# Kernel optimization log

Measured on AMD Instinct MI355X. Metric: run time of the kernel, lower is better.

## Reference

```python
import math
import jax, jax.numpy as jnp
import numpy as np

B, T, D_MODEL, H, D = 2, 1024, 1024, 16, 64
NUM_LEVELS = int(math.ceil(math.log2(T + 1))) + 1  # 12 for max_seq_len=1024


def _fenwick_level(idx):
    return (idx & -idx).bit_length() - 1


def build_fenwick_masks(T, num_levels):
    """NumPy replica of the torch build_fenwick_masks; returns [L, T, T] float32."""
    j_to_nodes = {}
    for j in range(1, T + 1):
        nodes = []
        idx = j
        while idx <= T:
            nodes.append((idx, _fenwick_level(idx)))
            idx += idx & -idx
        j_to_nodes[j] = nodes
    t_to_query_nodes = {}
    for t in range(1, T + 1):
        s = set()
        idx = t
        while idx > 0:
            s.add(idx)
            idx -= idx & -idx
        t_to_query_nodes[t] = s
    masks = np.zeros((num_levels, T, T), dtype=np.float32)
    for t in range(1, T + 1):
        qn = t_to_query_nodes[t]
        for j in range(1, t + 1):
            for node_idx, node_level in j_to_nodes[j]:
                if node_idx in qn:
                    masks[min(node_level, num_levels - 1), t - 1, j - 1] = 1.0
                    break
    return masks


def setup_inputs() -> dict:
    key = jax.random.key(0)
    ks = jax.random.split(key, 8)
    s = 0.02
    return {
        "x": jax.random.normal(ks[0], (B, T, D_MODEL), jnp.float32),
        "qw": jax.random.normal(ks[1], (D_MODEL, H * D), jnp.float32) * s,
        "qb": jnp.zeros((H * D,), jnp.float32),
        "kw": jax.random.normal(ks[2], (D_MODEL, H * D), jnp.float32) * s,
        "kb": jnp.zeros((H * D,), jnp.float32),
        "vw": jax.random.normal(ks[3], (D_MODEL, H * D), jnp.float32) * s,
        "vb": jnp.zeros((H * D,), jnp.float32),
        "lw": jax.random.normal(ks[4], (D_MODEL, H * NUM_LEVELS), jnp.float32) * s,
        "lb": jnp.zeros((H * NUM_LEVELS,), jnp.float32),
        "ow": jax.random.normal(ks[5], (H * D, D_MODEL), jnp.float32) * s,
        "ob": jnp.zeros((D_MODEL,), jnp.float32),
        "level_masks": jnp.asarray(build_fenwick_masks(T, NUM_LEVELS)),
    }


def reference(x, qw, qb, kw, kb, vw, vb, lw, lb, ow, ob, level_masks):
    b, t, _ = x.shape
    phi = lambda a: jax.nn.elu(a) + 1.0  # ELU+1 feature map
    # projections -> [B, H, T, D]
    Q = (x @ qw + qb).reshape(b, t, H, D).transpose(0, 2, 1, 3)
    K = (x @ kw + kb).reshape(b, t, H, D).transpose(0, 2, 1, 3)
    V = (x @ vw + vb).reshape(b, t, H, D).transpose(0, 2, 1, 3)
    Qp, Kp = phi(Q), phi(K)
    # per-level mixing weights: [B, H, T, L]
    logits = (x @ lw + lb).reshape(b, t, H, NUM_LEVELS).transpose(0, 2, 1, 3)
    w = jax.nn.softmax(logits, axis=-1)
    # scores are level-independent in the original; compute once
    S = jnp.einsum('bhid,bhjd->bhij', Qp, Kp)
    # sum_l w_l * mask_l folded into one weighted mask: [B, H, T, T]
    Mw = jnp.einsum('bhil,lij->bhij', w, level_masks)
    Sm = S * Mw
    num = jnp.einsum('bhij,bhjd->bhid', Sm, V)
    den = jnp.maximum(jnp.sum(Sm, axis=-1, keepdims=True), 1e-6)
    out = (num / den).transpose(0, 2, 1, 3).reshape(b, t, H * D)
    return out @ ow + ob
```

## Files before the change

kernel.cpp:

```cpp
#include <hip/hip_runtime.h>
#include <math.h>

typedef __bf16 bf16;
typedef __attribute__((ext_vector_type(4))) __bf16 bf16x4;
typedef __attribute__((ext_vector_type(8))) __bf16 bf16x8;
typedef __attribute__((ext_vector_type(4))) float f32x4;

#define B_SZ 2
#define T_SZ 1024
#define DM_SZ 1024
#define H_SZ 16
#define D_SZ 64
#define L_SZ 12
#define M_ROWS 2048
#define N_PAD 3328

__device__ __forceinline__ f32x4 mfma_16x16x32(bf16x8 a, bf16x8 b, f32x4 c) {
  return __builtin_amdgcn_mfma_f32_16x16x32_bf16(a, b, c, 0, 0, 0);
}

__device__ __forceinline__ void gload_lds16(const bf16* g, bf16* l) {
  __builtin_amdgcn_global_load_lds((const __attribute__((address_space(1))) void*)g,
                                   (__attribute__((address_space(3))) void*)l,
                                   16, 0, 0);
}

__global__ __launch_bounds__(256) void k_prep(
    const float* __restrict__ x, bf16* __restrict__ xb,
    const float* __restrict__ qw, const float* __restrict__ kw,
    const float* __restrict__ vw, const float* __restrict__ ow,
    const float* __restrict__ lw,
    bf16* __restrict__ wqkvT, bf16* __restrict__ owT) {
  const int z = blockIdx.z;
  const int t = threadIdx.x;
  if (z == 5) {
    const size_t base = ((size_t)blockIdx.y * 16 + blockIdx.x) * 8192 + t * 32;
#pragma unroll
    for (int u = 0; u < 4; ++u) {
      const float* p = x + base + u * 8;
      f32x4 a = *(const f32x4*)p;
      f32x4 b = *(const f32x4*)(p + 4);
      bf16x8 o;
#pragma unroll
      for (int e = 0; e < 4; ++e) { o[e] = (bf16)a[e]; o[e + 4] = (bf16)b[e]; }
      *(bf16x8*)(xb + base + u * 8) = o;
    }
    return;
  }
  __shared__ __align__(16) bf16 tile[64][66];
  const float* in; bf16* out; int C = 1024;
  if (z == 0)      { in = qw; out = wqkvT; }
  else if (z == 1) { in = kw; out = wqkvT + (size_t)1024 * DM_SZ; }
  else if (z == 2) { in = vw; out = wqkvT + (size_t)2048 * DM_SZ; }
  else if (z == 3) { in = ow; out = owT; }
  else             { in = lw; out = wqkvT + (size_t)3072 * DM_SZ; C = 192;
                     if (blockIdx.x >= 3) return; }
  const int tc = blockIdx.x * 64;
  const int tr = blockIdx.y * 64;
  const int r = t >> 2;
  const int c4 = (t & 3) << 4;
  const float* src = in + (size_t)(tr + r) * C + tc + c4;
  f32x4 f0 = *(const f32x4*)(src);
  f32x4 f1 = *(const f32x4*)(src + 4);
  f32x4 f2 = *(const f32x4*)(src + 8);
  f32x4 f3 = *(const f32x4*)(src + 12);
#pragma unroll
  for (int e = 0; e < 4; ++e) {
    tile[r][c4 + e]      = (bf16)f0[e];
    tile[r][c4 + 4 + e]  = (bf16)f1[e];
    tile[r][c4 + 8 + e]  = (bf16)f2[e];
    tile[r][c4 + 12 + e] = (bf16)f3[e];
  }
  __syncthreads();
  bf16x8 w0, w1;
#pragma unroll
  for (int e = 0; e < 8; ++e) { w0[e] = tile[c4 + e][r]; w1[e] = tile[c4 + 8 + e][r]; }
  bf16* dst = out + (size_t)(tc + r) * DM_SZ + tr + c4;
  *(bf16x8*)(dst) = w0;
  *(bf16x8*)(dst + 8) = w1;
}

__global__ __launch_bounds__(256) void k_gemm_qkvl(
    const bf16* __restrict__ A, const bf16* __restrict__ Wt,
    const float* __restrict__ qb, const float* __restrict__ kb,
    const float* __restrict__ vb, const float* __restrict__ lb,
    bf16* __restrict__ Qp, bf16* __restrict__ Kp,
    bf16* __restrict__ VTg, float* __restrict__ logit) {
  __shared__ __align__(16) char smem[34816];
  bf16* As = (bf16*)smem;
  bf16* Bs = As + 8192;
  const int nb = blockIdx.x * 128;
  const int mb = blockIdx.y * 128;
  const int t = threadIdx.x;
  const int wv = t >> 6;
  const int lane = t & 63;
  const int l16 = lane & 15;
  const int quad = lane >> 4;
  const int wm = (wv & 1) * 64;
  const int wn = (wv >> 1) * 64;

  const int trow = t >> 3;
  const int tcol = (t & 7) * 8;

  const f32x4 zero4 = {0.f, 0.f, 0.f, 0.f};
  f32x4 acc[4][4];
#pragma unroll
  for (int i = 0; i < 4; ++i)
#pragma unroll
    for (int j = 0; j < 4; ++j) acc[i][j] = zero4;

  const bf16* ag = A + (size_t)(mb + trow) * DM_SZ + tcol;
  const bf16* bg = Wt + (size_t)(nb + trow) * DM_SZ + tcol;

  for (int k0 = 0; k0 < DM_SZ; k0 += 64) {
    __syncthreads();
#pragma unroll
    for (int i = 0; i < 4; ++i)
      gload_lds16(ag + (size_t)i * 32 * DM_SZ + k0, As + i * 2048 + t * 8);
#pragma unroll
    for (int i = 0; i < 4; ++i)
      gload_lds16(bg + (size_t)i * 32 * DM_SZ + k0, Bs + i * 2048 + t * 8);
    __syncthreads();
#pragma unroll
    for (int ks = 0; ks < 2; ++ks) {
      bf16x8 af[4];
#pragma unroll
      for (int mi = 0; mi < 4; ++mi)
        af[mi] = *(const bf16x8*)(As + (wm + mi * 16 + l16) * 64 + ks * 32 + quad * 8);
#pragma unroll
      for (int ni = 0; ni < 4; ++ni) {
        bf16x8 bfr = *(const bf16x8*)(Bs + (wn + ni * 16 + l16) * 64 + ks * 32 + quad * 8);
#pragma unroll
        for (int mi = 0; mi < 4; ++mi)
          acc[mi][ni] = mfma_16x16x32(af[mi], bfr, acc[mi][ni]);
      }
    }
  }

  const int seg = nb >> 10;
  if (seg < 2) {
    const float* bias = seg == 0 ? qb : kb;
    bf16* outp = seg == 0 ? Qp : Kp;
    const int c0 = (nb & 1023) + wn;
#pragma unroll
    for (int ni = 0; ni < 4; ++ni) {
      const int col = c0 + ni * 16 + l16;
      const float bv = bias[col];
#pragma unroll
      for (int mi = 0; mi < 4; ++mi) {
#pragma unroll
        for (int r = 0; r < 4; ++r) {
          const int row = mb + wm + mi * 16 + quad * 4 + r;
          float v = acc[mi][ni][r] + bv;
          v = (v > 0.f) ? (v + 1.f) : __expf(v);
          outp[(size_t)row * DM_SZ + col] = (bf16)v;
        }
      }
    }
  } else if (seg == 2) {
    bf16* Trt = (bf16*)smem;
    const int cb = nb - 2048;
    __syncthreads();
#pragma unroll
    for (int ni = 0; ni < 4; ++ni) {
      const int nloc = wn + ni * 16 + l16;
      const float bv = vb[cb + nloc];
#pragma unroll
      for (int mi = 0; mi < 4; ++mi) {
        const int mloc = wm + mi * 16 + quad * 4;
        bf16x4 pk;
#pragma unroll
        for (int r = 0; r < 4; ++r) pk[r] = (bf16)(acc[mi][ni][r] + bv);
        *(bf16x4*)&Trt[nloc * 136 + mloc] = pk;
      }
    }
    __syncthreads();
    const int dn = t >> 1, ch = t & 1;
    const int bq = mb >> 10;
    const int m0g = mb & 1023;
    bf16* dst = VTg + ((size_t)(bq * 1024 + cb + dn)) * T_SZ + m0g + ch * 64;
    const bf16* srcl = Trt + dn * 136 + ch * 64;
#pragma unroll
    for (int e = 0; e < 8; ++e)
      *(bf16x8*)(dst + e * 8) = *(const bf16x8*)(srcl + e * 8);
  } else {
    const int lc0 = (nb - 3072) + wn;
#pragma unroll
    for (int ni = 0; ni < 4; ++ni) {
      const int lcol = lc0 + ni * 16 + l16;
      if (lcol < H_SZ * L_SZ) {
        const float bv = lb[lcol];
#pragma unroll
        for (int mi = 0; mi < 4; ++mi) {
#pragma unroll
          for (int r = 0; r < 4; ++r) {
            const int row = mb + wm + mi * 16 + quad * 4 + r;
            logit[(size_t)row * (H_SZ * L_SZ) + lcol] = acc[mi][ni][r] + bv;
          }
        }
      }
    }
  }
}

__global__ __launch_bounds__(256) void k_attn(const bf16* __restrict__ Qp,
                                              const bf16* __restrict__ Kp,
                                              const bf16* __restrict__ VTg,
                                              const float* __restrict__ Lg,
                                              bf16* __restrict__ O) {
  __shared__ __align__(16) bf16 Ks[64][80];
  __shared__ __align__(16) bf16 VTs[64][80];
  __shared__ __align__(16) bf16 Pl[4][16][80];
  __shared__ float Ws[64 * L_SZ];

  const int idx = blockIdx.x;
  const int s = idx >> 5;
  const int bh = idx & 31;
  const int it = (s < 8) ? (15 - s) : (s - 8);
  const int b = bh >> 4;
  const int h = bh & 15;
  const int i0 = it * 64;
  const int t = threadIdx.x;
  const int wv = t >> 6;
  const int lane = t & 63;
  const int l16 = lane & 15;
  const int quad = lane >> 4;
  const int m0 = wv * 16;

  const size_t base_bt = (size_t)b * T_SZ;

  const bf16* qptr = Qp + (base_bt + i0 + m0 + l16) * DM_SZ + h * 64 + quad * 8;
  const bf16x8 aq0 = *(const bf16x8*)(qptr);
  const bf16x8 aq1 = *(const bf16x8*)(qptr + 32);

  if (t < 64) {
    const float* lp = Lg + (base_bt + i0 + t) * (H_SZ * L_SZ) + h * L_SZ;
    float v[L_SZ];
    float m = -1e30f;
#pragma unroll
    for (int l = 0; l < L_SZ; ++l) { v[l] = lp[l]; m = fmaxf(m, v[l]); }
    float sum = 0.f;
#pragma unroll
    for (int l = 0; l < L_SZ; ++l) { v[l] = __expf(v[l] - m); sum += v[l]; }
    const float inv = 1.f / sum;
#pragma unroll
    for (int l = 0; l < L_SZ; ++l) Ws[t * L_SZ + l] = v[l] * inv;
  }

  const f32x4 zero4 = {0.f, 0.f, 0.f, 0.f};
  f32x4 accn[4];
#pragma unroll
  for (int tn = 0; tn < 4; ++tn) accn[tn] = zero4;
  float den[4] = {0.f, 0.f, 0.f, 0.f};

  const int sr = t >> 2;
  const int sc = (t & 3) << 4;
  const int il_base = m0 + quad * 4;

  const bf16* vtrow = VTg + ((size_t)bh * 64 + sr) * T_SZ;

  for (int jt = 0; jt <= it; ++jt) {
    const int j0 = jt * 64;
    const bf16* kpg = Kp + (base_bt + j0 + sr) * DM_SZ + h * 64 + sc;
    bf16x8 k0v = *(const bf16x8*)(kpg);
    bf16x8 k1v = *(const bf16x8*)(kpg + 8);
    const bf16* vpg = vtrow + j0 + sc;
    bf16x8 v0v = *(const bf16x8*)(vpg);
    bf16x8 v1v = *(const bf16x8*)(vpg + 8);
    __syncthreads();
    *(bf16x8*)&Ks[sr][sc] = k0v;
    *(bf16x8*)&Ks[sr][sc + 8] = k1v;
    *(bf16x8*)&VTs[sr][sc] = v0v;
    *(bf16x8*)&VTs[sr][sc + 8] = v1v;
    __syncthreads();

    f32x4 sacc[4];
#pragma unroll
    for (int tn = 0; tn < 4; ++tn) {
      sacc[tn] = zero4;
      bf16x8 bk0 = *(const bf16x8*)&Ks[tn * 16 + l16][quad * 8];
      bf16x8 bk1 = *(const bf16x8*)&Ks[tn * 16 + l16][32 + quad * 8];
      sacc[tn] = mfma_16x16x32(aq0, bk0, sacc[tn]);
      sacc[tn] = mfma_16x16x32(aq1, bk1, sacc[tn]);
    }

    if (jt < it) {
      const int lvlA = 6 + (31 - __clz((unsigned)(it ^ jt)));
      const int lvlB = 6 + (31 - __clz((unsigned)((it + 1) ^ jt)));
      float wrow[4];
#pragma unroll
      for (int r = 0; r < 4; ++r) {
        const int il = il_base + r;
        wrow[r] = Ws[il * L_SZ + ((il == 63) ? lvlB : lvlA)];
      }
#pragma unroll
      for (int tn = 0; tn < 4; ++tn) {
#pragma unroll
        for (int r = 0; r < 4; ++r) {
          const float p = sacc[tn][r] * wrow[r];
          den[r] += p;
          Pl[wv][quad * 4 + r][(tn * 16 + l16) ^ (quad << 4)] = (bf16)p;
        }
      }
    } else {
#pragma unroll
      for (int tn = 0; tn < 4; ++tn) {
#pragma unroll
        for (int r = 0; r < 4; ++r) {
          const int il = il_base + r;
          const int ig = i0 + il;
          const int jg = j0 + tn * 16 + l16;
          float p = 0.f;
          if (jg <= ig) {
            const int lvl = 31 - __clz((unsigned)((ig + 1) ^ jg));
            p = sacc[tn][r] * Ws[il * L_SZ + lvl];
          }
          den[r] += p;
          Pl[wv][quad * 4 + r][(tn * 16 + l16) ^ (quad << 4)] = (bf16)p;
        }
      }
    }

#pragma unroll
    for (int ks = 0; ks < 2; ++ks) {
      bf16x8 apf = *(const bf16x8*)&Pl[wv][l16][(ks * 32 + quad * 8) ^ ((l16 >> 2) << 4)];
#pragma unroll
      for (int tn = 0; tn < 4; ++tn) {
        bf16x8 bvf = *(const bf16x8*)&VTs[tn * 16 + l16][ks * 32 + quad * 8];
        accn[tn] = mfma_16x16x32(apf, bvf, accn[tn]);
      }
    }
  }

#pragma unroll
  for (int r = 0; r < 4; ++r) {
    float d = den[r];
    d += __shfl_xor(d, 1, 64);
    d += __shfl_xor(d, 2, 64);
    d += __shfl_xor(d, 4, 64);
    d += __shfl_xor(d, 8, 64);
    den[r] = fmaxf(d, 1e-6f);
  }

#pragma unroll
  for (int tn = 0; tn < 4; ++tn) {
#pragma unroll
    for (int r = 0; r < 4; ++r) {
      const int il = il_base + r;
      O[(base_bt + i0 + il) * DM_SZ + h * 64 + tn * 16 + l16] =
          (bf16)(accn[tn][r] / den[r]);
    }
  }
}

__global__ __launch_bounds__(256) void k_gemm_out(const bf16* __restrict__ A,
                                                  const bf16* __restrict__ Wt,
                                                  const float* __restrict__ ob,
                                                  float* __restrict__ out) {
  __shared__ __align__(16) bf16 As[64 * 64];
  __shared__ __align__(16) bf16 Bs[64 * 64];
  const int nb = blockIdx.x * 64;
  const int mb = blockIdx.y * 64;
  const int t = threadIdx.x;
  const int wv = t >> 6;
  const int lane = t & 63;
  const int l16 = lane & 15;
  const int quad = lane >> 4;
  const int wm = wv * 16;

  const int trow = t >> 3;
  const int tcol = (t & 7) * 8;

  const f32x4 zero4 = {0.f, 0.f, 0.f, 0.f};
  f32x4 acc[4];
#pragma unroll
  for (int j = 0; j < 4; ++j) acc[j] = zero4;

  const bf16* ag = A + (size_t)(mb + trow) * DM_SZ + tcol;
  const bf16* bg = Wt + (size_t)(nb + trow) * DM_SZ + tcol;

  for (int k0 = 0; k0 < DM_SZ; k0 += 64) {
    __syncthreads();
    gload_lds16(ag + k0, As + t * 8);
    gload_lds16(ag + (size_t)32 * DM_SZ + k0, As + 2048 + t * 8);
    gload_lds16(bg + k0, Bs + t * 8);
    gload_lds16(bg + (size_t)32 * DM_SZ + k0, Bs + 2048 + t * 8);
    __syncthreads();
#pragma unroll
    for (int ks = 0; ks < 2; ++ks) {
      bf16x8 af = *(const bf16x8*)(As + (wm + l16) * 64 + ks * 32 + quad * 8);
#pragma unroll
      for (int ni = 0; ni < 4; ++ni) {
        bf16x8 bfr = *(const bf16x8*)(Bs + (ni * 16 + l16) * 64 + ks * 32 + quad * 8);
        acc[ni] = mfma_16x16x32(af, bfr, acc[ni]);
      }
    }
  }
#pragma unroll
  for (int ni = 0; ni < 4; ++ni) {
    const int col = nb + ni * 16 + l16;
    const float bv = ob[col];
#pragma unroll
    for (int r = 0; r < 4; ++r) {
      const int row = mb + wm + quad * 4 + r;
      out[(size_t)row * DM_SZ + col] = acc[ni][r] + bv;
    }
  }
}

extern "C" void kernel_launch(void* const* d_in, const int* in_sizes, int n_in,
                              void* d_out, int out_size, void* d_ws, size_t ws_size,
                              hipStream_t stream) {
  (void)in_sizes; (void)n_in; (void)out_size; (void)ws_size;
  const float* x  = (const float*)d_in[0];
  const float* qw = (const float*)d_in[1];
  const float* qb = (const float*)d_in[2];
  const float* kw = (const float*)d_in[3];
  const float* kb = (const float*)d_in[4];
  const float* vw = (const float*)d_in[5];
  const float* vb = (const float*)d_in[6];
  const float* lw = (const float*)d_in[7];
  const float* lb = (const float*)d_in[8];
  const float* ow = (const float*)d_in[9];
  const float* ob = (const float*)d_in[10];

  char* ws = (char*)d_ws;
  size_t off = 0;
  auto alloc = [&](size_t bytes) -> char* {
    char* p = ws + off;
    off += (bytes + 255) & ~(size_t)255;
    return p;
  };
  bf16* xb     = (bf16*)alloc((size_t)M_ROWS * DM_SZ * 2);
  bf16* wqkvT  = (bf16*)alloc((size_t)N_PAD * DM_SZ * 2);
  bf16* owT    = (bf16*)alloc((size_t)DM_SZ * DM_SZ * 2);
  bf16* Qp     = (bf16*)alloc((size_t)M_ROWS * DM_SZ * 2);
  bf16* Kpb    = (bf16*)alloc((size_t)M_ROWS * DM_SZ * 2);
  bf16* VTg    = (bf16*)alloc((size_t)M_ROWS * DM_SZ * 2);
  bf16* attn   = (bf16*)alloc((size_t)M_ROWS * DM_SZ * 2);
  float* logit = (float*)alloc((size_t)M_ROWS * H_SZ * L_SZ * 4);

  const dim3 blk(256);
  k_prep<<<dim3(16, 16, 6), blk, 0, stream>>>(x, xb, qw, kw, vw, ow, lw, wqkvT, owT);
  k_gemm_qkvl<<<dim3(N_PAD / 128, M_ROWS / 128), blk, 0, stream>>>(
      xb, wqkvT, qb, kb, vb, lb, Qp, Kpb, VTg, logit);
  k_attn<<<dim3((T_SZ / 64) * B_SZ * H_SZ), blk, 0, stream>>>(Qp, Kpb, VTg, logit, attn);
  k_gemm_out<<<dim3(DM_SZ / 64, M_ROWS / 64), blk, 0, stream>>>(attn, owT, ob, (float*)d_out);
}
```

Before: 182.6 us.

## Fuse all stages into one cooperative persistent kernel with grid syncs

Merges the prep, QKV/logit GEMM, attention and output GEMM kernels into a single cooperative launch of 512 blocks, using grid.sync between phases and reusing one shared-memory buffer. The goal is to remove three kernel launch gaps and tail drains. The cost is that each phase is capped at 512 resident blocks, and work that was spread over more blocks is now looped or left idle (for example only 416 blocks run the GEMM). A fallback path launches the separate kernels if the cooperative launch fails.

```diff
diff --git a/kernel.cpp b/kernel.cpp
--- a/kernel.cpp
+++ b/kernel.cpp
@@ -1,5 +1,8 @@
 #include <hip/hip_runtime.h>
+#include <hip/hip_cooperative_groups.h>
 #include <math.h>
+
+namespace cg = cooperative_groups;
 
 typedef __bf16 bf16;
 typedef __attribute__((ext_vector_type(4))) __bf16 bf16x4;
@@ -14,6 +17,7 @@
 #define L_SZ 12
 #define M_ROWS 2048
 #define N_PAD 3328
+#define SMEM_BYTES 34816
 
 __device__ __forceinline__ f32x4 mfma_16x16x32(bf16x8 a, bf16x8 b, f32x4 c) {
   return __builtin_amdgcn_mfma_f32_16x16x32_bf16(a, b, c, 0, 0, 0);
@@ -25,40 +29,49 @@
                                    16, 0, 0);
 }
 
-__global__ __launch_bounds__(256) void k_prep(
-    const float* __restrict__ x, bf16* __restrict__ xb,
-    const float* __restrict__ qw, const float* __restrict__ kw,
-    const float* __restrict__ vw, const float* __restrict__ ow,
-    const float* __restrict__ lw,
-    bf16* __restrict__ wqkvT, bf16* __restrict__ owT) {
-  const int z = blockIdx.z;
-  const int t = threadIdx.x;
-  if (z == 5) {
-    const size_t base = ((size_t)blockIdx.y * 16 + blockIdx.x) * 8192 + t * 32;
-#pragma unroll
-    for (int u = 0; u < 4; ++u) {
-      const float* p = x + base + u * 8;
+struct Params {
+  const float *x, *qw, *kw, *vw, *ow, *lw;
+  const float *qb, *kb, *vb, *lb, *ob;
+  bf16 *xb, *wqkvT, *owT, *Qp, *Kp, *VTg, *attn;
+  float *logit;
+  float *out;
+};
+
+__device__ void prep_unit(int u, int t, char* smem, const Params& P) {
+  if (u >= 1328) return;
+  if (u >= 1072) {
+    const int cu = u - 1072;
+    const size_t base = (size_t)cu * 8192 + t * 32;
+#pragma unroll
+    for (int c = 0; c < 4; ++c) {
+      const float* p = P.x + base + c * 8;
       f32x4 a = *(const f32x4*)p;
       f32x4 b = *(const f32x4*)(p + 4);
       bf16x8 o;
 #pragma unroll
       for (int e = 0; e < 4; ++e) { o[e] = (bf16)a[e]; o[e + 4] = (bf16)b[e]; }
-      *(bf16x8*)(xb + base + u * 8) = o;
+      *(bf16x8*)(P.xb + base + c * 8) = o;
     }
     return;
   }
-  __shared__ __align__(16) bf16 tile[64][66];
-  const float* in; bf16* out; int C = 1024;
-  if (z == 0)      { in = qw; out = wqkvT; }
-  else if (z == 1) { in = kw; out = wqkvT + (size_t)1024 * DM_SZ; }
-  else if (z == 2) { in = vw; out = wqkvT + (size_t)2048 * DM_SZ; }
-  else if (z == 3) { in = ow; out = owT; }
-  else             { in = lw; out = wqkvT + (size_t)3072 * DM_SZ; C = 192;
-                     if (blockIdx.x >= 3) return; }
-  const int tc = blockIdx.x * 64;
-  const int tr = blockIdx.y * 64;
+  bf16 (*tile)[66] = (bf16(*)[66])smem;
+  const float* in; bf16* out; int C = 1024, tx, ty;
+  if (u < 1024) {
+    const int z = u >> 8, id = u & 255;
+    tx = id & 15; ty = id >> 4;
+    if (z == 0)      { in = P.qw; out = P.wqkvT; }
+    else if (z == 1) { in = P.kw; out = P.wqkvT + (size_t)1024 * DM_SZ; }
+    else if (z == 2) { in = P.vw; out = P.wqkvT + (size_t)2048 * DM_SZ; }
+    else             { in = P.ow; out = P.owT; }
+  } else {
+    const int id = u - 1024;
+    tx = id % 3; ty = id / 3;
+    in = P.lw; out = P.wqkvT + (size_t)3072 * DM_SZ; C = 192;
+  }
+  const int tc = tx * 64, tr = ty * 64;
   const int r = t >> 2;
   const int c4 = (t & 3) << 4;
+  __syncthreads();
   const float* src = in + (size_t)(tr + r) * C + tc + c4;
   f32x4 f0 = *(const f32x4*)(src);
   f32x4 f1 = *(const f32x4*)(src + 4);
@@ -80,25 +93,17 @@
   *(bf16x8*)(dst + 8) = w1;
 }
 
-__global__ __launch_bounds__(256) void k_gemm_qkvl(
-    const bf16* __restrict__ A, const bf16* __restrict__ Wt,
-    const float* __restrict__ qb, const float* __restrict__ kb,
-    const float* __restrict__ vb, const float* __restrict__ lb,
-    bf16* __restrict__ Qp, bf16* __restrict__ Kp,
-    bf16* __restrict__ VTg, float* __restrict__ logit) {
-  __shared__ __align__(16) char smem[34816];
+__device__ void qkvl_phase(int blk, int t, char* smem, const Params& P) {
   bf16* As = (bf16*)smem;
   bf16* Bs = As + 8192;
-  const int nb = blockIdx.x * 128;
-  const int mb = blockIdx.y * 128;
-  const int t = threadIdx.x;
+  const int nb = (blk % 26) * 128;
+  const int mb = (blk / 26) * 128;
   const int wv = t >> 6;
   const int lane = t & 63;
   const int l16 = lane & 15;
   const int quad = lane >> 4;
   const int wm = (wv & 1) * 64;
   const int wn = (wv >> 1) * 64;
-
   const int trow = t >> 3;
   const int tcol = (t & 7) * 8;
 
@@ -109,8 +114,8 @@
 #pragma unroll
     for (int j = 0; j < 4; ++j) acc[i][j] = zero4;
 
-  const bf16* ag = A + (size_t)(mb + trow) * DM_SZ + tcol;
-  const bf16* bg = Wt + (size_t)(nb + trow) * DM_SZ + tcol;
+  const bf16* ag = P.xb + (size_t)(mb + trow) * DM_SZ + tcol;
+  const bf16* bg = P.wqkvT + (size_t)(nb + trow) * DM_SZ + tcol;
 
   for (int k0 = 0; k0 < DM_SZ; k0 += 64) {
     __syncthreads();
@@ -139,8 +144,8 @@
 
   const int seg = nb >> 10;
   if (seg < 2) {
-    const float* bias = seg == 0 ? qb : kb;
-    bf16* outp = seg == 0 ? Qp : Kp;
+    const float* bias = seg == 0 ? P.qb : P.kb;
+    bf16* outp = seg == 0 ? P.Qp : P.Kp;
     const int c0 = (nb & 1023) + wn;
 #pragma unroll
     for (int ni = 0; ni < 4; ++ni) {
@@ -164,7 +169,7 @@
 #pragma unroll
     for (int ni = 0; ni < 4; ++ni) {
       const int nloc = wn + ni * 16 + l16;
-      const float bv = vb[cb + nloc];
+      const float bv = P.vb[cb + nloc];
 #pragma unroll
       for (int mi = 0; mi < 4; ++mi) {
         const int mloc = wm + mi * 16 + quad * 4;
@@ -178,7 +183,7 @@
     const int dn = t >> 1, ch = t & 1;
     const int bq = mb >> 10;
     const int m0g = mb & 1023;
-    bf16* dst = VTg + ((size_t)(bq * 1024 + cb + dn)) * T_SZ + m0g + ch * 64;
+    bf16* dst = P.VTg + ((size_t)(bq * 1024 + cb + dn)) * T_SZ + m0g + ch * 64;
     const bf16* srcl = Trt + dn * 136 + ch * 64;
 #pragma unroll
     for (int e = 0; e < 8; ++e)
@@ -189,13 +194,13 @@
     for (int ni = 0; ni < 4; ++ni) {
       const int lcol = lc0 + ni * 16 + l16;
       if (lcol < H_SZ * L_SZ) {
-        const float bv = lb[lcol];
+        const float bv = P.lb[lcol];
 #pragma unroll
         for (int mi = 0; mi < 4; ++mi) {
 #pragma unroll
           for (int r = 0; r < 4; ++r) {
             const int row = mb + wm + mi * 16 + quad * 4 + r;
-            logit[(size_t)row * (H_SZ * L_SZ) + lcol] = acc[mi][ni][r] + bv;
+            P.logit[(size_t)row * (H_SZ * L_SZ) + lcol] = acc[mi][ni][r] + bv;
           }
         }
       }
@@ -203,24 +208,18 @@
   }
 }
 
-__global__ __launch_bounds__(256) void k_attn(const bf16* __restrict__ Qp,
-                                              const bf16* __restrict__ Kp,
-                                              const bf16* __restrict__ VTg,
-                                              const float* __restrict__ Lg,
-                                              bf16* __restrict__ O) {
-  __shared__ __align__(16) bf16 Ks[64][80];
-  __shared__ __align__(16) bf16 VTs[64][80];
-  __shared__ __align__(16) bf16 Pl[4][16][80];
-  __shared__ float Ws[64 * L_SZ];
-
-  const int idx = blockIdx.x;
-  const int s = idx >> 5;
-  const int bh = idx & 31;
+__device__ void attn_phase(int blk, int t, char* smem, const Params& P) {
+  bf16 (*Ks)[80]  = (bf16(*)[80])(smem);
+  bf16 (*VTs)[80] = (bf16(*)[80])(smem + 10240);
+  bf16 (*Pl)[16][80] = (bf16(*)[16][80])(smem + 20480);
+  float* Ws = (float*)(smem + 30720);
+
+  const int s = blk >> 5;
+  const int bh = blk & 31;
   const int it = (s < 8) ? (15 - s) : (s - 8);
   const int b = bh >> 4;
   const int h = bh & 15;
   const int i0 = it * 64;
-  const int t = threadIdx.x;
   const int wv = t >> 6;
   const int lane = t & 63;
   const int l16 = lane & 15;
@@ -229,12 +228,12 @@
 
   const size_t base_bt = (size_t)b * T_SZ;
 
-  const bf16* qptr = Qp + (base_bt + i0 + m0 + l16) * DM_SZ + h * 64 + quad * 8;
+  const bf16* qptr = P.Qp + (base_bt + i0 + m0 + l16) * DM_SZ + h * 64 + quad * 8;
   const bf16x8 aq0 = *(const bf16x8*)(qptr);
   const bf16x8 aq1 = *(const bf16x8*)(qptr + 32);
 
   if (t < 64) {
-    const float* lp = Lg + (base_bt + i0 + t) * (H_SZ * L_SZ) + h * L_SZ;
+    const float* lp = P.logit + (base_bt + i0 + t) * (H_SZ * L_SZ) + h * L_SZ;
     float v[L_SZ];
     float m = -1e30f;
 #pragma unroll
@@ -257,11 +256,11 @@
   const int sc = (t & 3) << 4;
   const int il_base = m0 + quad * 4;
 
-  const bf16* vtrow = VTg + ((size_t)bh * 64 + sr) * T_SZ;
+  const bf16* vtrow = P.VTg + ((size_t)bh * 64 + sr) * T_SZ;
 
   for (int jt = 0; jt <= it; ++jt) {
     const int j0 = jt * 64;
-    const bf16* kpg = Kp + (base_bt + j0 + sr) * DM_SZ + h * 64 + sc;
+    const bf16* kpg = P.Kp + (base_bt + j0 + sr) * DM_SZ + h * 64 + sc;
     bf16x8 k0v = *(const bf16x8*)(kpg);
     bf16x8 k1v = *(const bf16x8*)(kpg + 8);
     const bf16* vpg = vtrow + j0 + sc;
@@ -347,27 +346,22 @@
 #pragma unroll
     for (int r = 0; r < 4; ++r) {
       const int il = il_base + r;
-      O[(base_bt + i0 + il) * DM_SZ + h * 64 + tn * 16 + l16] =
+      P.attn[(base_bt + i0 + il) * DM_SZ + h * 64 + tn * 16 + l16] =
           (bf16)(accn[tn][r] / den[r]);
     }
   }
 }
 
-__global__ __launch_bounds__(256) void k_gemm_out(const bf16* __restrict__ A,
-                                                  const bf16* __restrict__ Wt,
-                                                  const float* __restrict__ ob,
-                                                  float* __restrict__ out) {
-  __shared__ __align__(16) bf16 As[64 * 64];
-  __shared__ __align__(16) bf16 Bs[64 * 64];
-  const int nb = blockIdx.x * 64;
-  const int mb = blockIdx.y * 64;
-  const int t = threadIdx.x;
+__device__ void out_phase(int blk, int t, char* smem, const Params& P) {
+  bf16* As = (bf16*)smem;
+  bf16* Bs = As + 4096;
+  const int nb = (blk & 15) * 64;
+  const int mb = (blk >> 4) * 64;
   const int wv = t >> 6;
   const int lane = t & 63;
   const int l16 = lane & 15;
   const int quad = lane >> 4;
   const int wm = wv * 16;
-
   const int trow = t >> 3;
   const int tcol = (t & 7) * 8;
 
@@ -376,8 +370,8 @@
 #pragma unroll
   for (int j = 0; j < 4; ++j) acc[j] = zero4;
 
-  const bf16* ag = A + (size_t)(mb + trow) * DM_SZ + tcol;
-  const bf16* bg = Wt + (size_t)(nb + trow) * DM_SZ + tcol;
+  const bf16* ag = P.attn + (size_t)(mb + trow) * DM_SZ + tcol;
+  const bf16* bg = P.owT + (size_t)(nb + trow) * DM_SZ + tcol;
 
   for (int k0 = 0; k0 < DM_SZ; k0 += 64) {
     __syncthreads();
@@ -399,31 +393,53 @@
 #pragma unroll
   for (int ni = 0; ni < 4; ++ni) {
     const int col = nb + ni * 16 + l16;
-    const float bv = ob[col];
+    const float bv = P.ob[col];
 #pragma unroll
     for (int r = 0; r < 4; ++r) {
       const int row = mb + wm + quad * 4 + r;
-      out[(size_t)row * DM_SZ + col] = acc[ni][r] + bv;
-    }
-  }
+      P.out[(size_t)row * DM_SZ + col] = acc[ni][r] + bv;
+    }
+  }
+}
+
+__global__ __launch_bounds__(256, 2) void k_mega(Params P) {
+  __shared__ __align__(16) char smem[SMEM_BYTES];
+  cg::grid_group grid = cg::this_grid();
+  const int blk = blockIdx.x;
+  const int t = threadIdx.x;
+
+#pragma unroll
+  for (int u3 = 0; u3 < 3; ++u3) prep_unit(u3 * 512 + blk, t, smem, P);
+  grid.sync();
+  if (blk < 416) qkvl_phase(blk, t, smem, P);
+  grid.sync();
+  attn_phase(blk, t, smem, P);
+  grid.sync();
+  out_phase(blk, t, smem, P);
+}
+
+__global__ __launch_bounds__(256) void k_prep_sa(Params P) {
+  __shared__ __align__(16) char smem[8448];
+  const int u = blockIdx.x;
+  prep_unit(u, threadIdx.x, smem, P);
+}
+__global__ __launch_bounds__(256) void k_qkvl_sa(Params P) {
+  __shared__ __align__(16) char smem[SMEM_BYTES];
+  qkvl_phase(blockIdx.x, threadIdx.x, smem, P);
+}
+__global__ __launch_bounds__(256) void k_attn_sa(Params P) {
+  __shared__ __align__(16) char smem[33792];
+  attn_phase(blockIdx.x, threadIdx.x, smem, P);
+}
+__global__ __launch_bounds__(256) void k_out_sa(Params P) {
+  __shared__ __align__(16) char smem[16384];
+  out_phase(blockIdx.x, threadIdx.x, smem, P);
 }
 
 extern "C" void kernel_launch(void* const* d_in, const int* in_sizes, int n_in,
                               void* d_out, int out_size, void* d_ws, size_t ws_size,
                               hipStream_t stream) {
   (void)in_sizes; (void)n_in; (void)out_size; (void)ws_size;
-  const float* x  = (const float*)d_in[0];
-  const float* qw = (const float*)d_in[1];
-  const float* qb = (const float*)d_in[2];
-  const float* kw = (const float*)d_in[3];
-  const float* kb = (const float*)d_in[4];
-  const float* vw = (const float*)d_in[5];
-  const float* vb = (const float*)d_in[6];
-  const float* lw = (const float*)d_in[7];
-  const float* lb = (const float*)d_in[8];
-  const float* ow = (const float*)d_in[9];
-  const float* ob = (const float*)d_in[10];
-
   char* ws = (char*)d_ws;
   size_t off = 0;
   auto alloc = [&](size_t bytes) -> char* {
@@ -431,19 +447,35 @@
     off += (bytes + 255) & ~(size_t)255;
     return p;
   };
-  bf16* xb     = (bf16*)alloc((size_t)M_ROWS * DM_SZ * 2);
-  bf16* wqkvT  = (bf16*)alloc((size_t)N_PAD * DM_SZ * 2);
-  bf16* owT    = (bf16*)alloc((size_t)DM_SZ * DM_SZ * 2);
-  bf16* Qp     = (bf16*)alloc((size_t)M_ROWS * DM_SZ * 2);
-  bf16* Kpb    = (bf16*)alloc((size_t)M_ROWS * DM_SZ * 2);
-  bf16* VTg    = (bf16*)alloc((size_t)M_ROWS * DM_SZ * 2);
-  bf16* attn   = (bf16*)alloc((size_t)M_ROWS * DM_SZ * 2);
-  float* logit = (float*)alloc((size_t)M_ROWS * H_SZ * L_SZ * 4);
-
-  const dim3 blk(256);
-  k_prep<<<dim3(16, 16, 6), blk, 0, stream>>>(x, xb, qw, kw, vw, ow, lw, wqkvT, owT);
-  k_gemm_qkvl<<<dim3(N_PAD / 128, M_ROWS / 128), blk, 0, stream>>>(
-      xb, wqkvT, qb, kb, vb, lb, Qp, Kpb, VTg, logit);
-  k_attn<<<dim3((T_SZ / 64) * B_SZ * H_SZ), blk, 0, stream>>>(Qp, Kpb, VTg, logit, attn);
-  k_gemm_out<<<dim3(DM_SZ / 64, M_ROWS / 64), blk, 0, stream>>>(attn, owT, ob, (float*)d_out);
-}
+  Params p;
+  p.x  = (const float*)d_in[0];
+  p.qw = (const float*)d_in[1];
+  p.qb = (const float*)d_in[2];
+  p.kw = (const float*)d_in[3];
+  p.kb = (const float*)d_in[4];
+  p.vw = (const float*)d_in[5];
+  p.vb = (const float*)d_in[6];
+  p.lw = (const float*)d_in[7];
+  p.lb = (const float*)d_in[8];
+  p.ow = (const float*)d_in[9];
+  p.ob = (const float*)d_in[10];
+  p.xb     = (bf16*)alloc((size_t)M_ROWS * DM_SZ * 2);
+  p.wqkvT  = (bf16*)alloc((size_t)N_PAD * DM_SZ * 2);
+  p.owT    = (bf16*)alloc((size_t)DM_SZ * DM_SZ * 2);
+  p.Qp     = (bf16*)alloc((size_t)M_ROWS * DM_SZ * 2);
+  p.Kp     = (bf16*)alloc((size_t)M_ROWS * DM_SZ * 2);
+  p.VTg    = (bf16*)alloc((size_t)M_ROWS * DM_SZ * 2);
+  p.attn   = (bf16*)alloc((size_t)M_ROWS * DM_SZ * 2);
+  p.logit  = (float*)alloc((size_t)M_ROWS * H_SZ * L_SZ * 4);
+  p.out    = (float*)d_out;
+
+  void* kargs[] = {(void*)&p};
+  hipError_t e = hipLaunchCooperativeKernel((const void*)k_mega, dim3(512),
+                                            dim3(256), kargs, 0, stream);
+  if (e != hipSuccess) {
+    k_prep_sa<<<dim3(1328), dim3(256), 0, stream>>>(p);
+    k_qkvl_sa<<<dim3(416), dim3(256), 0, stream>>>(p);
+    k_attn_sa<<<dim3(512), dim3(256), 0, stream>>>(p);
+    k_out_sa<<<dim3(512), dim3(256), 0, stream>>>(p);
+  }
+}
```

After: 416.7 us. 128% more time.

## Compact prep grid, overlap ow transpose with QKV GEMM, async K/V LDS loads

Applied to the files above, without the earlier changes.

The prep kernel now uses a 1-D grid that launches only the blocks it needs, instead of a 6-plane grid where many lw blocks exit early. The ow transpose moves out of prep into 96 extra blocks of the QKV GEMM launch, so it runs alongside the GEMM tiles. The attention kernel now loads K and V tiles with direct global-to-LDS loads into unpadded 64-wide buffers, replacing register staging. The unpadded layout may bring back LDS bank conflicts on the MFMA operand reads.

```diff
diff --git a/kernel.cpp b/kernel.cpp
--- a/kernel.cpp
+++ b/kernel.cpp
@@ -28,35 +28,37 @@
 __global__ __launch_bounds__(256) void k_prep(
     const float* __restrict__ x, bf16* __restrict__ xb,
     const float* __restrict__ qw, const float* __restrict__ kw,
-    const float* __restrict__ vw, const float* __restrict__ ow,
-    const float* __restrict__ lw,
-    bf16* __restrict__ wqkvT, bf16* __restrict__ owT) {
-  const int z = blockIdx.z;
+    const float* __restrict__ vw, const float* __restrict__ lw,
+    bf16* __restrict__ wqkvT) {
+  const int u = blockIdx.x;
   const int t = threadIdx.x;
-  if (z == 5) {
-    const size_t base = ((size_t)blockIdx.y * 16 + blockIdx.x) * 8192 + t * 32;
-#pragma unroll
-    for (int u = 0; u < 4; ++u) {
-      const float* p = x + base + u * 8;
+  if (u >= 816) {
+    const size_t base = (size_t)(u - 816) * 8192 + t * 32;
+#pragma unroll
+    for (int c = 0; c < 4; ++c) {
+      const float* p = x + base + c * 8;
       f32x4 a = *(const f32x4*)p;
       f32x4 b = *(const f32x4*)(p + 4);
       bf16x8 o;
 #pragma unroll
       for (int e = 0; e < 4; ++e) { o[e] = (bf16)a[e]; o[e + 4] = (bf16)b[e]; }
-      *(bf16x8*)(xb + base + u * 8) = o;
+      *(bf16x8*)(xb + base + c * 8) = o;
     }
     return;
   }
   __shared__ __align__(16) bf16 tile[64][66];
-  const float* in; bf16* out; int C = 1024;
-  if (z == 0)      { in = qw; out = wqkvT; }
-  else if (z == 1) { in = kw; out = wqkvT + (size_t)1024 * DM_SZ; }
-  else if (z == 2) { in = vw; out = wqkvT + (size_t)2048 * DM_SZ; }
-  else if (z == 3) { in = ow; out = owT; }
-  else             { in = lw; out = wqkvT + (size_t)3072 * DM_SZ; C = 192;
-                     if (blockIdx.x >= 3) return; }
-  const int tc = blockIdx.x * 64;
-  const int tr = blockIdx.y * 64;
+  const float* in; bf16* out; int C = 1024, tx, ty;
+  if (u < 768) {
+    const int z = u >> 8, id = u & 255;
+    tx = id & 15; ty = id >> 4;
+    in = z == 0 ? qw : z == 1 ? kw : vw;
+    out = wqkvT + (size_t)z * 1024 * DM_SZ;
+  } else {
+    const int id = u - 768;
+    tx = id % 3; ty = id / 3;
+    in = lw; out = wqkvT + (size_t)3072 * DM_SZ; C = 192;
+  }
+  const int tc = tx * 64, tr = ty * 64;
   const int r = t >> 2;
   const int c4 = (t & 3) << 4;
   const float* src = in + (size_t)(tr + r) * C + tc + c4;
@@ -84,21 +86,53 @@
     const bf16* __restrict__ A, const bf16* __restrict__ Wt,
     const float* __restrict__ qb, const float* __restrict__ kb,
     const float* __restrict__ vb, const float* __restrict__ lb,
+    const float* __restrict__ ow, bf16* __restrict__ owT,
     bf16* __restrict__ Qp, bf16* __restrict__ Kp,
     bf16* __restrict__ VTg, float* __restrict__ logit) {
   __shared__ __align__(16) char smem[34816];
+  const int blk = blockIdx.x;
+  const int t = threadIdx.x;
+
+  if (blk >= 416) {
+    bf16 (*tile)[66] = (bf16(*)[66])smem;
+    const int r = t >> 2;
+    const int c4 = (t & 3) << 4;
+    for (int u = blk - 416; u < 256; u += 96) {
+      const int tc = (u & 15) * 64, tr = (u >> 4) * 64;
+      __syncthreads();
+      const float* src = ow + (size_t)(tr + r) * DM_SZ + tc + c4;
+      f32x4 f0 = *(const f32x4*)(src);
+      f32x4 f1 = *(const f32x4*)(src + 4);
+      f32x4 f2 = *(const f32x4*)(src + 8);
+      f32x4 f3 = *(const f32x4*)(src + 12);
+#pragma unroll
+      for (int e = 0; e < 4; ++e) {
+        tile[r][c4 + e]      = (bf16)f0[e];
+        tile[r][c4 + 4 + e]  = (bf16)f1[e];
+        tile[r][c4 + 8 + e]  = (bf16)f2[e];
+        tile[r][c4 + 12 + e] = (bf16)f3[e];
+      }
+      __syncthreads();
+      bf16x8 w0, w1;
+#pragma unroll
+      for (int e = 0; e < 8; ++e) { w0[e] = tile[c4 + e][r]; w1[e] = tile[c4 + 8 + e][r]; }
+      bf16* dst = owT + (size_t)(tc + r) * DM_SZ + tr + c4;
+      *(bf16x8*)(dst) = w0;
+      *(bf16x8*)(dst + 8) = w1;
+    }
+    return;
+  }
+
   bf16* As = (bf16*)smem;
   bf16* Bs = As + 8192;
-  const int nb = blockIdx.x * 128;
-  const int mb = blockIdx.y * 128;
-  const int t = threadIdx.x;
+  const int nb = (blk % 26) * 128;
+  const int mb = (blk / 26) * 128;
   const int wv = t >> 6;
   const int lane = t & 63;
   const int l16 = lane & 15;
   const int quad = lane >> 4;
   const int wm = (wv & 1) * 64;
   const int wn = (wv >> 1) * 64;
-
   const int trow = t >> 3;
   const int tcol = (t & 7) * 8;
 
@@ -208,8 +242,8 @@
                                               const bf16* __restrict__ VTg,
                                               const float* __restrict__ Lg,
                                               bf16* __restrict__ O) {
-  __shared__ __align__(16) bf16 Ks[64][80];
-  __shared__ __align__(16) bf16 VTs[64][80];
+  __shared__ __align__(16) bf16 Ks[64 * 64];
+  __shared__ __align__(16) bf16 VTs[64 * 64];
   __shared__ __align__(16) bf16 Pl[4][16][80];
   __shared__ float Ws[64 * L_SZ];
 
@@ -253,33 +287,28 @@
   for (int tn = 0; tn < 4; ++tn) accn[tn] = zero4;
   float den[4] = {0.f, 0.f, 0.f, 0.f};
 
-  const int sr = t >> 2;
-  const int sc = (t & 3) << 4;
   const int il_base = m0 + quad * 4;
-
-  const bf16* vtrow = VTg + ((size_t)bh * 64 + sr) * T_SZ;
+  const int srow = t >> 3;
+  const int scol = (t & 7) * 8;
+
+  const bf16* kbase = Kp + (base_bt + srow) * DM_SZ + h * 64 + scol;
+  const bf16* vbase = VTg + ((size_t)bh * 64 + srow) * T_SZ + scol;
 
   for (int jt = 0; jt <= it; ++jt) {
     const int j0 = jt * 64;
-    const bf16* kpg = Kp + (base_bt + j0 + sr) * DM_SZ + h * 64 + sc;
-    bf16x8 k0v = *(const bf16x8*)(kpg);
-    bf16x8 k1v = *(const bf16x8*)(kpg + 8);
-    const bf16* vpg = vtrow + j0 + sc;
-    bf16x8 v0v = *(const bf16x8*)(vpg);
-    bf16x8 v1v = *(const bf16x8*)(vpg + 8);
-    __syncthreads();
-    *(bf16x8*)&Ks[sr][sc] = k0v;
-    *(bf16x8*)&Ks[sr][sc + 8] = k1v;
-    *(bf16x8*)&VTs[sr][sc] = v0v;
-    *(bf16x8*)&VTs[sr][sc + 8] = v1v;
+    __syncthreads();
+    gload_lds16(kbase + (size_t)j0 * DM_SZ, Ks + t * 8);
+    gload_lds16(kbase + (size_t)(j0 + 32) * DM_SZ, Ks + 2048 + t * 8);
+    gload_lds16(vbase + j0, VTs + t * 8);
+    gload_lds16(vbase + (size_t)32 * T_SZ + j0, VTs + 2048 + t * 8);
     __syncthreads();
 
     f32x4 sacc[4];
 #pragma unroll
     for (int tn = 0; tn < 4; ++tn) {
       sacc[tn] = zero4;
-      bf16x8 bk0 = *(const bf16x8*)&Ks[tn * 16 + l16][quad * 8];
-      bf16x8 bk1 = *(const bf16x8*)&Ks[tn * 16 + l16][32 + quad * 8];
+      bf16x8 bk0 = *(const bf16x8*)(Ks + (tn * 16 + l16) * 64 + quad * 8);
+      bf16x8 bk1 = *(const bf16x8*)(Ks + (tn * 16 + l16) * 64 + 32 + quad * 8);
       sacc[tn] = mfma_16x16x32(aq0, bk0, sacc[tn]);
       sacc[tn] = mfma_16x16x32(aq1, bk1, sacc[tn]);
     }
@@ -326,7 +355,7 @@
       bf16x8 apf = *(const bf16x8*)&Pl[wv][l16][(ks * 32 + quad * 8) ^ ((l16 >> 2) << 4)];
 #pragma unroll
       for (int tn = 0; tn < 4; ++tn) {
-        bf16x8 bvf = *(const bf16x8*)&VTs[tn * 16 + l16][ks * 32 + quad * 8];
+        bf16x8 bvf = *(const bf16x8*)(VTs + (tn * 16 + l16) * 64 + ks * 32 + quad * 8);
         accn[tn] = mfma_16x16x32(apf, bvf, accn[tn]);
       }
     }
@@ -359,15 +388,14 @@
                                                   float* __restrict__ out) {
   __shared__ __align__(16) bf16 As[64 * 64];
   __shared__ __align__(16) bf16 Bs[64 * 64];
-  const int nb = blockIdx.x * 64;
-  const int mb = blockIdx.y * 64;
+  const int nb = (blockIdx.x & 15) * 64;
+  const int mb = (blockIdx.x >> 4) * 64;
   const int t = threadIdx.x;
   const int wv = t >> 6;
   const int lane = t & 63;
   const int l16 = lane & 15;
   const int quad = lane >> 4;
   const int wm = wv * 16;
-
   const int trow = t >> 3;
   const int tcol = (t & 7) * 8;
 
@@ -441,9 +469,9 @@
   float* logit = (float*)alloc((size_t)M_ROWS * H_SZ * L_SZ * 4);
 
   const dim3 blk(256);
-  k_prep<<<dim3(16, 16, 6), blk, 0, stream>>>(x, xb, qw, kw, vw, ow, lw, wqkvT, owT);
-  k_gemm_qkvl<<<dim3(N_PAD / 128, M_ROWS / 128), blk, 0, stream>>>(
-      xb, wqkvT, qb, kb, vb, lb, Qp, Kpb, VTg, logit);
+  k_prep<<<dim3(1072), blk, 0, stream>>>(x, xb, qw, kw, vw, lw, wqkvT);
+  k_gemm_qkvl<<<dim3(512), blk, 0, stream>>>(
+      xb, wqkvT, qb, kb, vb, lb, ow, owT, Qp, Kpb, VTg, logit);
   k_attn<<<dim3((T_SZ / 64) * B_SZ * H_SZ), blk, 0, stream>>>(Qp, Kpb, VTg, logit, attn);
-  k_gemm_out<<<dim3(DM_SZ / 64, M_ROWS / 64), blk, 0, stream>>>(attn, owT, ob, (float*)d_out);
-}
+  k_gemm_out<<<dim3(512), blk, 0, stream>>>(attn, owT, ob, (float*)d_out);
+}
```

Measured after the change: 184.2 us. About the same (+0.9%).
